# Kernel optimization log

Hardware: AMD Instinct MI355X
Metric: run time of the kernel (lower is better)

Reference implementation:

```python
import jax, jax.numpy as jnp
import numpy as np

G, P, DEG = 1024, 75, 8            # graphs, nodes per graph, out-degree
N, E = G * P, G * P * DEG
KS, DIM = 5, 2
K = KS ** DIM                      # 25 spline weight matrices
VOX = 4                            # 2x2 voxel grid per graph (size=14 over [0,27.99])


def setup_inputs():
    key = jax.random.key(0)
    ks = jax.random.split(key, 14)
    x = jax.random.uniform(ks[0], (N, 1), dtype=jnp.float32)            # pixel intensities
    src = jnp.repeat(jnp.arange(N, dtype=jnp.int32), DEG)
    dst = (src // P) * P + jax.random.randint(ks[1], (E,), 0, P, dtype=jnp.int32)
    edge_index = jnp.stack([src, dst])                                   # [2,E], within-graph edges
    edge_attr = jax.random.uniform(ks[2], (E, DIM), dtype=jnp.float32)  # Cartesian pseudo-coords in [0,1]
    batch = jnp.repeat(jnp.arange(G, dtype=jnp.int32), P)
    pos = jax.random.uniform(ks[3], (N, DIM), dtype=jnp.float32) * 27.99

    def nrm(k, shape, fan_in):
        return jax.random.normal(k, shape, jnp.float32) / np.float32(np.sqrt(fan_in))

    W1 = nrm(ks[4], (K, 1, 32), 1.0)
    root1 = nrm(ks[5], (1, 32), 1.0)
    b1 = jnp.zeros((32,), jnp.float32)
    W2 = nrm(ks[6], (K, 32, 64), 32.0)
    root2 = nrm(ks[7], (32, 64), 32.0)
    b2 = jnp.zeros((64,), jnp.float32)
    W3 = nrm(ks[8], (K, 64, 64), 64.0)
    root3 = nrm(ks[9], (64, 64), 64.0)
    b3 = jnp.zeros((64,), jnp.float32)
    fc1_w = nrm(ks[10], (4 * 64, 128), 256.0)
    fc1_b = jnp.zeros((128,), jnp.float32)
    fc2_w = nrm(ks[11], (128, 10), 128.0)
    fc2_b = jnp.zeros((10,), jnp.float32)
    return dict(x=x, edge_index=edge_index, edge_attr=edge_attr, batch=batch, pos=pos,
                W1=W1, root1=root1, b1=b1, W2=W2, root2=root2, b2=b2,
                W3=W3, root3=root3, b3=b3,
                fc1_w=fc1_w, fc1_b=fc1_b, fc2_w=fc2_w, fc2_b=fc2_b)


def spline_basis(u):
    """Degree-1 open B-spline basis, dim=2, kernel_size=5. u:[E,2] in [0,1].
    Returns basis [E,4] and flat weight indices [E,4]."""
    p = u * (KS - 1)
    lo = jnp.clip(jnp.floor(p), 0.0, KS - 1)
    frac = p - lo
    lo_i = lo.astype(jnp.int32)
    hi_i = jnp.minimum(lo_i + 1, KS - 1)
    w0 = jnp.stack([1.0 - frac[:, 0], frac[:, 0]], 1)   # [E,2]
    w1 = jnp.stack([1.0 - frac[:, 1], frac[:, 1]], 1)
    i0 = jnp.stack([lo_i[:, 0], hi_i[:, 0]], 1)
    i1 = jnp.stack([lo_i[:, 1], hi_i[:, 1]], 1)
    basis = (w0[:, :, None] * w1[:, None, :]).reshape(-1, 4)      # [E,4]
    idx = (i0[:, :, None] + KS * i1[:, None, :]).reshape(-1, 4)   # [E,4]
    return basis, idx


def spline_conv(h, src, dst, basis, idx, W, root, bias):
    # per-node transform under all K kernel weights: [N,K,O]
    y = jnp.einsum('ni,kio->nko', h, W)
    O = W.shape[2]
    msg = jnp.zeros((src.shape[0], O), h.dtype)
    for s in range(4):  # 4 B-spline corner contributions (fixed small loop)
        msg = msg + basis[:, s:s + 1] * y[src, idx[:, s]]
    agg = jax.ops.segment_sum(msg, dst, num_segments=N)
    deg = jax.ops.segment_sum(jnp.ones((src.shape[0],), h.dtype), dst, num_segments=N)
    agg = agg / jnp.maximum(deg, 1.0)[:, None]          # aggr='mean'
    return agg + h @ root + bias


def reference(x, edge_index, edge_attr, batch, pos,
              W1, root1, b1, W2, root2, b2, W3, root3, b3,
              fc1_w, fc1_b, fc2_w, fc2_b):
    src, dst = edge_index[0], edge_index[1]
    basis, idx = spline_basis(edge_attr)
    h = jax.nn.elu(spline_conv(x, src, dst, basis, idx, W1, root1, b1))
    h = jax.nn.elu(spline_conv(h, src, dst, basis, idx, W2, root2, b2))
    h = jax.nn.elu(spline_conv(h, src, dst, basis, idx, W3, root3, b3))
    # voxel_grid(size=14, start=0, end=27.99) -> 2x2 grid per graph
    vox = jnp.clip((pos / 14.0).astype(jnp.int32), 0, 1)          # [N,2]
    cluster = batch * VOX + vox[:, 0] + 2 * vox[:, 1]
    pooled = jax.ops.segment_max(h, cluster, num_segments=G * VOX)
    pooled = jnp.where(jnp.isneginf(pooled), 0.0, pooled)         # empty voxels -> 0
    graph_x = pooled.reshape(G, VOX * 64)                          # [G, 256]
    graph_x = jax.nn.elu(graph_x @ fc1_w + fc1_b)                  # dropout: eval mode (identity)
    logits = graph_x @ fc2_w + fc2_b
    return jax.nn.log_softmax(logits, axis=1)
```

## Files before the change

### kernel.cpp

```cpp
#include <hip/hip_runtime.h>
#include <math.h>

#define NG 1024
#define NP 75
#define NE_G 600
#define E_TOT 614400
#define NK 25
#define NSEG 1875
#define SST 104
#define YTST 104
#define HST 72

typedef _Float16 half8 __attribute__((ext_vector_type(8)));
typedef float floatx4 __attribute__((ext_vector_type(4)));

#define WS_WT2 0
#define WS_WT3 51200
#define WS_R2T 153600
#define WS_R3T 155648

__device__ __forceinline__ float elu_f(float x) {
    return x > 0.f ? x : (expf(x) - 1.f);
}
__device__ __forceinline__ float h16f(unsigned short b) {
    union { unsigned short u; _Float16 h; } c; c.u = b; return (float)c.h;
}
__device__ __forceinline__ _Float16 bits16(unsigned short b) {
    union { unsigned short u; _Float16 h; } c; c.u = b; return c.h;
}
__device__ __forceinline__ unsigned short f16bits(float v) {
    union { _Float16 h; unsigned short u; } c; c.h = (_Float16)v; return c.u;
}

__global__ void __launch_bounds__(256) prep_weights(
    const float* __restrict__ W2, const float* __restrict__ root2,
    const float* __restrict__ W3, const float* __restrict__ root3,
    _Float16* __restrict__ ws)
{
    int i = blockIdx.x * 256 + threadIdx.x;
    int stride = gridDim.x * 256;
    for (int t = i; t < 25 * 64 * 32; t += stride) {
        int k = t >> 11, o = (t >> 5) & 63, ci = t & 31;
        ws[WS_WT2 + t] = (_Float16)W2[(k * 32 + ci) * 64 + o];
    }
    for (int t = i; t < 25 * 64 * 64; t += stride) {
        int k = t >> 12, o = (t >> 6) & 63, ci = t & 63;
        ws[WS_WT3 + t] = (_Float16)W3[(k * 64 + ci) * 64 + o];
    }
    for (int t = i; t < 64 * 32; t += stride) {
        int o = t >> 5, ci = t & 31;
        ws[WS_R2T + t] = (_Float16)root2[ci * 64 + o];
    }
    for (int t = i; t < 64 * 64; t += stride) {
        int o = t >> 6, ci = t & 63;
        ws[WS_R3T + t] = (_Float16)root3[ci * 64 + o];
    }
}

struct EdgeB { int dl; int kk[4]; unsigned short bas[4]; };
__device__ __forceinline__ EdgeB edge_basis(const float* __restrict__ attr,
                                            const int* __restrict__ eidx,
                                            int g, int e) {
    EdgeB r;
    int ge = g * NE_G + e;
    r.dl = eidx[E_TOT + ge] - g * NP;
    float p0 = attr[2 * ge + 0] * 4.f, p1 = attr[2 * ge + 1] * 4.f;
    float fl0 = fminf(fmaxf(floorf(p0), 0.f), 4.f);
    float fl1 = fminf(fmaxf(floorf(p1), 0.f), 4.f);
    float fr0 = p0 - fl0, fr1 = p1 - fl1;
    int i00 = (int)fl0, i10 = (int)fl1;
    int i01 = min(i00 + 1, 4), i11 = min(i10 + 1, 4);
    float w0a[2] = {1.f - fr0, fr0};
    float w1a[2] = {1.f - fr1, fr1};
    int i0a[2] = {i00, i01};
    int i1a[2] = {i10, i11};
    #pragma unroll
    for (int a = 0; a < 2; ++a)
        #pragma unroll
        for (int b = 0; b < 2; ++b) {
            int s = a * 2 + b;
            r.kk[s] = i0a[a] + 5 * i1a[b];
            r.bas[s] = f16bits(w0a[a] * w1a[b]);
        }
    return r;
}

template<int CIN>
__device__ __forceinline__ void conv_layer(
    const _Float16* __restrict__ Wt,
    const _Float16* __restrict__ rootT,
    const float* __restrict__ bias,
    _Float16* __restrict__ sb_S,
    _Float16* __restrict__ sb_yT,
    _Float16* __restrict__ sb_h,
    const unsigned* __restrict__ sb_list,
    const int* __restrict__ sb_koff,
    const float* __restrict__ sb_rdeg,
    int tid, int lane, int wid)
{
    const int m = lane & 15, q = (lane >> 4) & 3;
    const int o = wid * 16 + m;
    constexpr int KK = CIN / 32;

    half8 Ah[5][KK];
    #pragma unroll
    for (int mt = 0; mt < 5; ++mt)
        #pragma unroll
        for (int kk = 0; kk < KK; ++kk)
            Ah[mt][kk] = *(const half8*)&sb_h[(mt * 16 + m) * HST + kk * 32 + q * 8];
    __syncthreads();

    floatx4 agg[5];
    #pragma unroll
    for (int mt = 0; mt < 5; ++mt) agg[mt] = (floatx4){0.f, 0.f, 0.f, 0.f};

    half8 Bc[KK], Bn[KK];
    #pragma unroll
    for (int kk = 0; kk < KK; ++kk)
        Bc[kk] = *(const half8*)&Wt[(0 * 64 + o) * CIN + kk * 32 + q * 8];

    for (int k = 0; k < NK; ++k) {
        const int jb = sb_koff[k] + tid, kend = sb_koff[k + 1];
        unsigned upre = (jb < kend) ? sb_list[jb] : 0u;
        const _Float16* nb = (k < NK - 1) ? &Wt[((k + 1) * 64 + o) * CIN]
                                          : &rootT[o * CIN];
        #pragma unroll
        for (int kk = 0; kk < KK; ++kk)
            Bn[kk] = *(const half8*)&nb[kk * 32 + q * 8];
        for (int t = tid; t < 80 * SST / 8; t += 256)
            ((floatx4*)sb_S)[t] = (floatx4){0.f, 0.f, 0.f, 0.f};
        #pragma unroll
        for (int mt = 0; mt < 5; ++mt) {
            floatx4 c = {0.f, 0.f, 0.f, 0.f};
            #pragma unroll
            for (int kk = 0; kk < KK; ++kk)
                c = __builtin_amdgcn_mfma_f32_16x16x32_f16(Ah[mt][kk], Bc[kk], c, 0, 0, 0);
            union { _Float16 h[4]; unsigned long long u64; } p;
            p.h[0] = (_Float16)c[0]; p.h[1] = (_Float16)c[1];
            p.h[2] = (_Float16)c[2]; p.h[3] = (_Float16)c[3];
            *(unsigned long long*)&sb_yT[o * YTST + mt * 16 + q * 4] = p.u64;
        }
        __syncthreads();
        {
            bool first = true;
            for (int j = jb; j < kend; j += 256) {
                unsigned u = first ? upre : sb_list[j];
                first = false;
                if (u >> 16)
                    sb_S[((u >> 7) & 127) * SST + (u & 127)] = bits16((unsigned short)(u >> 16));
            }
        }
        __syncthreads();
        {
            half8 B0 = *(const half8*)&sb_yT[o * YTST + 0 + q * 8];
            half8 B1 = *(const half8*)&sb_yT[o * YTST + 32 + q * 8];
            half8 B2 = *(const half8*)&sb_yT[o * YTST + 64 + q * 8];
            #pragma unroll
            for (int mt = 0; mt < 5; ++mt) {
                half8 a0 = *(const half8*)&sb_S[(mt * 16 + m) * SST + 0 + q * 8];
                half8 a1 = *(const half8*)&sb_S[(mt * 16 + m) * SST + 32 + q * 8];
                half8 a2 = *(const half8*)&sb_S[(mt * 16 + m) * SST + 64 + q * 8];
                floatx4 c = agg[mt];
                c = __builtin_amdgcn_mfma_f32_16x16x32_f16(a0, B0, c, 0, 0, 0);
                c = __builtin_amdgcn_mfma_f32_16x16x32_f16(a1, B1, c, 0, 0, 0);
                c = __builtin_amdgcn_mfma_f32_16x16x32_f16(a2, B2, c, 0, 0, 0);
                agg[mt] = c;
            }
        }
        #pragma unroll
        for (int kk = 0; kk < KK; ++kk) Bc[kk] = Bn[kk];
        __syncthreads();
    }

    float bo = bias[o];
    #pragma unroll
    for (int mt = 0; mt < 5; ++mt) {
        floatx4 c = {0.f, 0.f, 0.f, 0.f};
        #pragma unroll
        for (int kk = 0; kk < KK; ++kk)
            c = __builtin_amdgcn_mfma_f32_16x16x32_f16(Ah[mt][kk], Bc[kk], c, 0, 0, 0);
        #pragma unroll
        for (int r = 0; r < 4; ++r) {
            int n = mt * 16 + q * 4 + r;
            if (n < NP) {
                float v = agg[mt][r] * sb_rdeg[n] + c[r] + bo;
                sb_h[n * HST + o] = (_Float16)elu_f(v);
            }
        }
    }
    for (int p = tid; p < 5 * HST / 2; p += 256)
        ((unsigned*)&sb_h[NP * HST])[p] = 0u;
    __syncthreads();
}

__global__ void __launch_bounds__(256, 4) mnist_spline_fused(
    const float* __restrict__ xg,
    const int* __restrict__ eidx,
    const float* __restrict__ attr,
    const float* __restrict__ pos,
    const float* __restrict__ W1, const float* __restrict__ root1, const float* __restrict__ b1,
    const float* __restrict__ b2, const float* __restrict__ b3,
    const float* __restrict__ fc1w, const float* __restrict__ fc1b,
    const float* __restrict__ fc2w, const float* __restrict__ fc2b,
    const _Float16* __restrict__ ws,
    float* __restrict__ out)
{
    const int g = blockIdx.x;
    const int tid = threadIdx.x;
    const int lane = tid & 63;
    const int wid = tid >> 6;

    __shared__ __align__(16) unsigned char sb_SU[80 * SST * 2];
    __shared__ __align__(16) _Float16 sb_yT[64 * YTST];
    __shared__ __align__(16) unsigned sb_list[NE_G * 4];
    __shared__ int sb_koff[26];
    __shared__ float sb_x[80];
    __shared__ float sb_rdeg[80];
    __shared__ int sb_deg[80];
    __shared__ unsigned sb_vmask[12];
    __shared__ unsigned sb_wsum[8];

    _Float16* sb_S = (_Float16*)sb_SU;
    _Float16* sb_h = (_Float16*)sb_SU;
    unsigned* cnt32 = (unsigned*)sb_SU;
    unsigned short* segoff = (unsigned short*)(sb_SU + 11520);
    _Float16* T1 = (_Float16*)sb_SU;
    _Float16* W1T = (_Float16*)sb_yT;
    float* fc_gx = (float*)(sb_SU + 11776);
    float* fc_part = (float*)(sb_SU + 12800);
    float* fc_z1 = (float*)(sb_SU + 14848);

    for (int p = tid; p < 80; p += 256) sb_deg[p] = 0;
    for (int p = tid; p < NSEG; p += 256) cnt32[p] = 0u;
    for (int p = tid; p < 5 * HST / 2; p += 256)
        ((unsigned*)&sb_h[NP * HST])[p] = 0u;
    for (int p = tid; p < 64 * 12; p += 256) {
        int ch = p / 12, c = p % 12;
        ((unsigned*)sb_yT)[ch * (YTST / 2) + 40 + c] = 0u;
    }
    if (tid < 12) sb_vmask[tid] = 0u;
    __syncthreads();
    for (int p = tid; p < 32 * 32; p += 256) {
        int k = p >> 5, o = p & 31;
        W1T[o * 32 + k] = (k < NK) ? (_Float16)W1[k * 32 + o] : (_Float16)0.f;
    }

    for (int e = tid; e < NE_G; e += 256) {
        EdgeB eb = edge_basis(attr, eidx, g, e);
        atomicAdd(&sb_deg[eb.dl], 1);
        #pragma unroll
        for (int s = 0; s < 4; ++s)
            atomicAdd(&cnt32[eb.kk[s] * NP + eb.dl], 1u);
    }
    for (int n = tid; n < NP; n += 256) {
        int gn = g * NP + n;
        sb_x[n] = xg[gn];
        int v0 = min(max((int)(pos[2 * gn] * (1.f / 14.f)), 0), 1);
        int v1 = min(max((int)(pos[2 * gn + 1] * (1.f / 14.f)), 0), 1);
        int v = v0 + 2 * v1;
        atomicOr(&sb_vmask[v * 3 + (n >> 5)], 1u << (n & 31));
    }
    __syncthreads();

    {
        int base = tid * 8;
        unsigned c8[8], lsum = 0;
        #pragma unroll
        for (int i = 0; i < 8; ++i) {
            int idx = base + i;
            c8[i] = (idx < NSEG) ? cnt32[idx] : 0u;
            lsum += c8[i];
        }
        unsigned v = lsum;
        #pragma unroll
        for (int d = 1; d < 64; d <<= 1) {
            unsigned ov = __shfl_up(v, d);
            if (lane >= d) v += ov;
        }
        if (lane == 63) sb_wsum[wid] = v;
        __syncthreads();
        unsigned wpre = 0;
        for (int w2 = 0; w2 < wid; ++w2) wpre += sb_wsum[w2];
        unsigned run = wpre + v - lsum;
        #pragma unroll
        for (int i = 0; i < 8; ++i) {
            int idx = base + i;
            if (idx < NSEG + 1) segoff[idx] = (unsigned short)run;
            if (idx < NSEG) cnt32[idx] = run;
            run += c8[i];
        }
        if (tid < 80) sb_rdeg[tid] = (tid < NP) ? 1.f / fmaxf((float)sb_deg[tid], 1.f) : 0.f;
    }
    __syncthreads();

    for (int e = tid; e < NE_G; e += 256) {
        EdgeB eb = edge_basis(attr, eidx, g, e);
        int srcl = e >> 3;
        #pragma unroll
        for (int s = 0; s < 4; ++s) {
            unsigned p = atomicAdd(&cnt32[eb.kk[s] * NP + eb.dl], 1u);
            sb_list[p] = ((unsigned)eb.bas[s] << 16) | ((unsigned)eb.dl << 7) | (unsigned)srcl;
        }
    }
    if (tid < 26) sb_koff[tid] = segoff[min(tid * NP, NSEG)];
    __syncthreads();

    for (int s = tid; s < NSEG; s += 256) {
        int s0 = segoff[s], s1 = segoff[s + 1];
        float tsum = 0.f;
        for (int j = s0; j < s1; ++j) {
            unsigned u = sb_list[j];
            if (!(u >> 16)) continue;
            int src = u & 127;
            float bsum = h16f((unsigned short)(u >> 16));
            for (int j2 = j + 1; j2 < s1; ++j2) {
                unsigned u2 = sb_list[j2];
                if ((u2 & 127) == (unsigned)src && (u2 >> 16)) {
                    bsum += h16f((unsigned short)(u2 >> 16));
                    sb_list[j2] = u2 & 0xFFFFu;
                }
            }
            sb_list[j] = ((unsigned)f16bits(bsum) << 16) | (u & 0xFFFFu);
            tsum += bsum * sb_x[src];
        }
        int k = s / NP, d = s - k * NP;
        T1[d * 40 + k] = (_Float16)tsum;
    }
    for (int t = tid; t < NP * 15 + 5 * 40; t += 256) {
        int d, k;
        if (t < NP * 15) { d = t / 15; k = NK + t % 15; }
        else { int t2 = t - NP * 15; d = NP + t2 / 40; k = t2 % 40; }
        T1[d * 40 + k] = (_Float16)0.f;
    }
    __syncthreads();

    {
        floatx4 l1c[5];
        const int m = lane & 15, q = (lane >> 4) & 3;
        const int o = wid * 16 + m;
        if (wid < 2) {
            half8 Bw = *(const half8*)&W1T[o * 32 + q * 8];
            #pragma unroll
            for (int mt = 0; mt < 5; ++mt) {
                half8 a = *(const half8*)&T1[(mt * 16 + m) * 40 + q * 8];
                floatx4 c = {0.f, 0.f, 0.f, 0.f};
                l1c[mt] = __builtin_amdgcn_mfma_f32_16x16x32_f16(a, Bw, c, 0, 0, 0);
            }
        }
        __syncthreads();
        if (wid < 2) {
            float rt = root1[o], bo = b1[o];
            #pragma unroll
            for (int mt = 0; mt < 5; ++mt)
                #pragma unroll
                for (int r = 0; r < 4; ++r) {
                    int n = mt * 16 + q * 4 + r;
                    if (n < NP) {
                        float v = l1c[mt][r] * sb_rdeg[n] + sb_x[n] * rt + bo;
                        sb_h[n * HST + o] = (_Float16)elu_f(v);
                    }
                }
        }
    }
    __syncthreads();

    conv_layer<32>(ws + WS_WT2, ws + WS_R2T, b2, sb_S, sb_yT, sb_h,
                   sb_list, sb_koff, sb_rdeg, tid, lane, wid);
    conv_layer<64>(ws + WS_WT3, ws + WS_R3T, b3, sb_S, sb_yT, sb_h,
                   sb_list, sb_koff, sb_rdeg, tid, lane, wid);

    {
        int v = wid, o = lane;
        float mval = -INFINITY;
        #pragma unroll 25
        for (int n = 0; n < NP; ++n) {
            float val = (float)sb_h[n * HST + o];
            bool sel = (sb_vmask[v * 3 + (n >> 5)] >> (n & 31)) & 1;
            mval = sel ? fmaxf(mval, val) : mval;
        }
        fc_gx[v * 64 + o] = (mval == -INFINITY) ? 0.f : mval;
    }
    __syncthreads();

    {
        float acc0 = 0.f, acc1 = 0.f;
        #pragma unroll 8
        for (int i = 0; i < 64; ++i) {
            int ii = wid * 64 + i;
            float xv = fc_gx[ii];
            acc0 += xv * fc1w[ii * 128 + lane];
            acc1 += xv * fc1w[ii * 128 + 64 + lane];
        }
        fc_part[wid * 128 + lane] = acc0;
        fc_part[wid * 128 + 64 + lane] = acc1;
    }
    __syncthreads();
    if (tid < 128) {
        float v = fc_part[tid] + fc_part[128 + tid] + fc_part[256 + tid] + fc_part[384 + tid]
                + fc1b[tid];
        fc_z1[tid] = elu_f(v);
    }
    __syncthreads();

    if (wid == 0) {
        int o = lane & 15, sg = lane >> 4;
        float acc = 0.f;
        if (o < 10) {
            #pragma unroll 8
            for (int i = sg * 32; i < sg * 32 + 32; ++i)
                acc += fc_z1[i] * fc2w[i * 10 + o];
        }
        acc += __shfl_xor(acc, 16);
        acc += __shfl_xor(acc, 32);
        float logit = (o < 10) ? (acc + fc2b[o]) : 0.f;
        float lv = (o < 10) ? logit : -INFINITY;
        float mx = lv;
        #pragma unroll
        for (int d = 1; d < 16; d <<= 1) mx = fmaxf(mx, __shfl_xor(mx, d));
        float ex = (o < 10) ? expf(logit - mx) : 0.f;
        float se = ex;
        #pragma unroll
        for (int d = 1; d < 16; d <<= 1) se += __shfl_xor(se, d);
        if (lane < 10) out[g * 10 + lane] = logit - mx - logf(se);
    }
}

extern "C" void kernel_launch(void* const* d_in, const int* in_sizes, int n_in,
                              void* d_out, int out_size, void* d_ws, size_t ws_size,
                              hipStream_t stream) {
    const float* xg    = (const float*)d_in[0];
    const int*   eidx  = (const int*)d_in[1];
    const float* attr  = (const float*)d_in[2];
    const float* pos   = (const float*)d_in[4];
    const float* W1    = (const float*)d_in[5];
    const float* root1 = (const float*)d_in[6];
    const float* b1    = (const float*)d_in[7];
    const float* W2    = (const float*)d_in[8];
    const float* root2 = (const float*)d_in[9];
    const float* b2    = (const float*)d_in[10];
    const float* W3    = (const float*)d_in[11];
    const float* root3 = (const float*)d_in[12];
    const float* b3    = (const float*)d_in[13];
    const float* fc1w  = (const float*)d_in[14];
    const float* fc1b  = (const float*)d_in[15];
    const float* fc2w  = (const float*)d_in[16];
    const float* fc2b  = (const float*)d_in[17];
    float* out = (float*)d_out;
    _Float16* ws = (_Float16*)d_ws;

    prep_weights<<<160, 256, 0, stream>>>(W2, root2, W3, root3, ws);
    mnist_spline_fused<<<NG, 256, 0, stream>>>(
        xg, eidx, attr, pos, W1, root1, b1, b2, b3,
        fc1w, fc1b, fc2w, fc2b, ws, out);
}
```

Before: 230.4 us.

## Redistribute aggregation MFMAs by row tile and merge scatter into projection phase

The edge-weight scatter into the sparse S tile now runs in the same phase as the per-kernel projection, which removes one block barrier per spline kernel index. The aggregation MFMAs are re-partitioned so each wave owns node-row tiles across all output channel tiles. Each wave then zeroes only its own S rows, and the root-weight product is computed at the end straight from global memory. In exchange, wave 3 handles two row tiles while the others handle one, which creates imbalance. The runtime-indexed Ah[MT] register array may also force dynamic indexing or scratch use.

```diff
diff --git a/kernel.cpp b/kernel.cpp
--- a/kernel.cpp
+++ b/kernel.cpp
@@ -101,6 +101,7 @@
     const int m = lane & 15, q = (lane >> 4) & 3;
     const int o = wid * 16 + m;
     constexpr int KK = CIN / 32;
+    const int nrt = (wid == 3) ? 2 : 1;
 
     half8 Ah[5][KK];
     #pragma unroll
@@ -110,25 +111,36 @@
             Ah[mt][kk] = *(const half8*)&sb_h[(mt * 16 + m) * HST + kk * 32 + q * 8];
     __syncthreads();
 
-    floatx4 agg[5];
+    for (int t = tid; t < 80 * SST / 8; t += 256)
+        ((floatx4*)sb_S)[t] = (floatx4){0.f, 0.f, 0.f, 0.f};
+
+    floatx4 agg[2][4];
     #pragma unroll
-    for (int mt = 0; mt < 5; ++mt) agg[mt] = (floatx4){0.f, 0.f, 0.f, 0.f};
+    for (int t = 0; t < 2; ++t)
+        #pragma unroll
+        for (int j = 0; j < 4; ++j) agg[t][j] = (floatx4){0.f, 0.f, 0.f, 0.f};
 
     half8 Bc[KK], Bn[KK];
     #pragma unroll
     for (int kk = 0; kk < KK; ++kk)
         Bc[kk] = *(const half8*)&Wt[(0 * 64 + o) * CIN + kk * 32 + q * 8];
+    __syncthreads();
 
     for (int k = 0; k < NK; ++k) {
-        const int jb = sb_koff[k] + tid, kend = sb_koff[k + 1];
-        unsigned upre = (jb < kend) ? sb_list[jb] : 0u;
-        const _Float16* nb = (k < NK - 1) ? &Wt[((k + 1) * 64 + o) * CIN]
-                                          : &rootT[o * CIN];
-        #pragma unroll
-        for (int kk = 0; kk < KK; ++kk)
-            Bn[kk] = *(const half8*)&nb[kk * 32 + q * 8];
-        for (int t = tid; t < 80 * SST / 8; t += 256)
-            ((floatx4*)sb_S)[t] = (floatx4){0.f, 0.f, 0.f, 0.f};
+        {
+            const int jb = sb_koff[k] + tid, kend = sb_koff[k + 1];
+            for (int j = jb; j < kend; j += 256) {
+                unsigned u = sb_list[j];
+                if (u >> 16)
+                    sb_S[((u >> 7) & 127) * SST + (u & 127)] = bits16((unsigned short)(u >> 16));
+            }
+        }
+        if (k < NK - 1) {
+            const _Float16* nb = &Wt[((k + 1) * 64 + o) * CIN];
+            #pragma unroll
+            for (int kk = 0; kk < KK; ++kk)
+                Bn[kk] = *(const half8*)&nb[kk * 32 + q * 8];
+        }
         #pragma unroll
         for (int mt = 0; mt < 5; ++mt) {
             floatx4 c = {0.f, 0.f, 0.f, 0.f};
@@ -141,55 +153,58 @@
             *(unsigned long long*)&sb_yT[o * YTST + mt * 16 + q * 4] = p.u64;
         }
         __syncthreads();
-        {
-            bool first = true;
-            for (int j = jb; j < kend; j += 256) {
-                unsigned u = first ? upre : sb_list[j];
-                first = false;
-                if (u >> 16)
-                    sb_S[((u >> 7) & 127) * SST + (u & 127)] = bits16((unsigned short)(u >> 16));
-            }
-        }
-        __syncthreads();
-        {
-            half8 B0 = *(const half8*)&sb_yT[o * YTST + 0 + q * 8];
-            half8 B1 = *(const half8*)&sb_yT[o * YTST + 32 + q * 8];
-            half8 B2 = *(const half8*)&sb_yT[o * YTST + 64 + q * 8];
-            #pragma unroll
-            for (int mt = 0; mt < 5; ++mt) {
-                half8 a0 = *(const half8*)&sb_S[(mt * 16 + m) * SST + 0 + q * 8];
-                half8 a1 = *(const half8*)&sb_S[(mt * 16 + m) * SST + 32 + q * 8];
-                half8 a2 = *(const half8*)&sb_S[(mt * 16 + m) * SST + 64 + q * 8];
-                floatx4 c = agg[mt];
+        #pragma unroll
+        for (int t = 0; t < 2; ++t) {
+            if (t == 1 && wid != 3) break;
+            const int MT = (wid < 3) ? wid : (3 + t);
+            half8 a0 = *(const half8*)&sb_S[(MT * 16 + m) * SST + 0 + q * 8];
+            half8 a1 = *(const half8*)&sb_S[(MT * 16 + m) * SST + 32 + q * 8];
+            half8 a2 = *(const half8*)&sb_S[(MT * 16 + m) * SST + 64 + q * 8];
+            #pragma unroll
+            for (int j = 0; j < 4; ++j) {
+                half8 B0 = *(const half8*)&sb_yT[(j * 16 + m) * YTST + 0 + q * 8];
+                half8 B1 = *(const half8*)&sb_yT[(j * 16 + m) * YTST + 32 + q * 8];
+                half8 B2 = *(const half8*)&sb_yT[(j * 16 + m) * YTST + 64 + q * 8];
+                floatx4 c = agg[t][j];
                 c = __builtin_amdgcn_mfma_f32_16x16x32_f16(a0, B0, c, 0, 0, 0);
                 c = __builtin_amdgcn_mfma_f32_16x16x32_f16(a1, B1, c, 0, 0, 0);
                 c = __builtin_amdgcn_mfma_f32_16x16x32_f16(a2, B2, c, 0, 0, 0);
-                agg[mt] = c;
-            }
-        }
-        #pragma unroll
-        for (int kk = 0; kk < KK; ++kk) Bc[kk] = Bn[kk];
+                agg[t][j] = c;
+            }
+            floatx4* zp = (floatx4*)&sb_S[MT * 16 * SST];
+            for (int i = lane; i < 16 * SST / 8; i += 64)
+                zp[i] = (floatx4){0.f, 0.f, 0.f, 0.f};
+        }
+        if (k < NK - 1) {
+            #pragma unroll
+            for (int kk = 0; kk < KK; ++kk) Bc[kk] = Bn[kk];
+        }
         __syncthreads();
     }
 
-    float bo = bias[o];
     #pragma unroll
-    for (int mt = 0; mt < 5; ++mt) {
-        floatx4 c = {0.f, 0.f, 0.f, 0.f};
-        #pragma unroll
-        for (int kk = 0; kk < KK; ++kk)
-            c = __builtin_amdgcn_mfma_f32_16x16x32_f16(Ah[mt][kk], Bc[kk], c, 0, 0, 0);
-        #pragma unroll
-        for (int r = 0; r < 4; ++r) {
-            int n = mt * 16 + q * 4 + r;
-            if (n < NP) {
-                float v = agg[mt][r] * sb_rdeg[n] + c[r] + bo;
-                sb_h[n * HST + o] = (_Float16)elu_f(v);
-            }
-        }
-    }
-    for (int p = tid; p < 5 * HST / 2; p += 256)
-        ((unsigned*)&sb_h[NP * HST])[p] = 0u;
+    for (int t = 0; t < 2; ++t) {
+        if (t == 1 && wid != 3) break;
+        const int MT = (wid < 3) ? wid : (3 + t);
+        #pragma unroll
+        for (int j = 0; j < 4; ++j) {
+            floatx4 c = {0.f, 0.f, 0.f, 0.f};
+            #pragma unroll
+            for (int kk = 0; kk < KK; ++kk) {
+                half8 rb = *(const half8*)&rootT[(j * 16 + m) * CIN + kk * 32 + q * 8];
+                c = __builtin_amdgcn_mfma_f32_16x16x32_f16(Ah[MT][kk], rb, c, 0, 0, 0);
+            }
+            float bo = bias[j * 16 + m];
+            #pragma unroll
+            for (int r = 0; r < 4; ++r) {
+                int n = MT * 16 + q * 4 + r;
+                if (n < NP) {
+                    float v = agg[t][j][r] * sb_rdeg[n] + c[r] + bo;
+                    sb_h[n * HST + (j * 16 + m)] = (_Float16)elu_f(v);
+                }
+            }
+        }
+    }
     __syncthreads();
 }
 
```

New measurement: 372.1 us. 1.62x slower.
